# Optimization experiments

Measured on AMD Instinct MI355X. Metric: run time of the kernel, lower is better.

## Reference

```python
import jax, jax.numpy as jnp
import numpy as np

P = 8192  # num_particles
C = 8192  # num EEG channels (must equal P for the original broadcast to be valid)


def setup_inputs() -> dict:
    key = jax.random.key(0)
    k1, k2, k3, k4, k5 = jax.random.split(key, 5)
    inputs = jax.random.normal(k1, (1, C, P), dtype=jnp.float32)
    state_vector = jax.random.normal(k2, (P, 3), dtype=jnp.float32)
    # near-identity transition for numerical sanity
    transition_matrix = jnp.eye(3, dtype=jnp.float32) + 0.01 * jax.random.normal(k3, (3, 3), dtype=jnp.float32)
    # symmetric positive-definite process noise covariance (Cholesky must succeed)
    a = jax.random.normal(k4, (3, 3), dtype=jnp.float32)
    process_noise_cov = 0.01 * (a @ a.T) + 0.1 * jnp.eye(3, dtype=jnp.float32)
    forward_matrix = jax.random.normal(k5, (C, 3), dtype=jnp.float32)
    return {
        "inputs": inputs,
        "state_vector": state_vector,
        "transition_matrix": transition_matrix,
        "process_noise_cov": process_noise_cov,
        "forward_matrix": forward_matrix,
    }


def reference(inputs, state_vector, transition_matrix, process_noise_cov, forward_matrix):
    k_noise, k_cat = jax.random.split(jax.random.key(42))
    # --- state transition: x_new = x @ T^T + eps,  eps ~ N(0, Q) via z @ chol(Q) ---
    updated = state_vector @ transition_matrix.T                      # (P, 3)
    L = jnp.linalg.cholesky(process_noise_cov)                        # (3, 3) lower
    z = jax.random.normal(k_noise, (P, 3), dtype=state_vector.dtype)
    state = updated + z @ L                                           # (P, 3)
    # --- EEG measurement model: H @ x^T -> (C, P) ---
    predicted = forward_matrix @ state.T                              # (C, P)
    # --- particle weights: squared-residual sum (broadcast (1,C,P) - (P,C), C==P) ---
    w = jnp.sum(jnp.square(inputs - predicted.T), axis=-1)[0]         # (P,)
    # --- categorical resampling on log-weights (unnormalized logits) ---
    idx = jax.random.categorical(k_cat, jnp.log(w), shape=(P,))       # (P,) int
    resampled = state[idx]                                            # (P, 3) gather
    return jnp.mean(resampled, axis=0)                                # (3,)
```

## Files before the change

### kernel.cpp

```cpp
#include <hip/hip_runtime.h>
#include <stdint.h>

#define NP 8192
#define NC 8192

__host__ __device__ inline uint32_t rotl32(uint32_t x, int r) {
  return (x << r) | (x >> (32 - r));
}

__host__ __device__ inline void threefry2x32(uint32_t k0, uint32_t k1,
                                             uint32_t x0, uint32_t x1,
                                             uint32_t& o0, uint32_t& o1) {
  uint32_t ks2 = k0 ^ k1 ^ 0x1BD11BDAu;
  x0 += k0; x1 += k1;
#define TF_R(r) { x0 += x1; x1 = rotl32(x1, (r)); x1 ^= x0; }
  TF_R(13) TF_R(15) TF_R(26) TF_R(6)   x0 += k1;  x1 += ks2 + 1u;
  TF_R(17) TF_R(29) TF_R(16) TF_R(24)  x0 += ks2; x1 += k0 + 2u;
  TF_R(13) TF_R(15) TF_R(26) TF_R(6)   x0 += k0;  x1 += k1 + 3u;
  TF_R(17) TF_R(29) TF_R(16) TF_R(24)  x0 += k1;  x1 += ks2 + 4u;
  TF_R(13) TF_R(15) TF_R(26) TF_R(6)   x0 += ks2; x1 += k0 + 5u;
#undef TF_R
  o0 = x0; o1 = x1;
}

__device__ inline uint32_t tf_bits(uint32_t k0, uint32_t k1, uint32_t i) {
  uint32_t o0, o1;
  threefry2x32(k0, k1, 0u, i, o0, o1);
  return o0 ^ o1;
}

__device__ inline float u01(uint32_t bits) {
  return __uint_as_float((bits >> 9) | 0x3f800000u) - 1.0f;
}

__device__ inline float erfinvf_(float x) {
  float w = -log1pf(-x * x);
  float p;
  if (w < 5.0f) {
    w -= 2.5f;
    p = 2.81022636e-08f;
    p = fmaf(p, w, 3.43273939e-07f);
    p = fmaf(p, w, -3.5233877e-06f);
    p = fmaf(p, w, -4.39150654e-06f);
    p = fmaf(p, w, 0.00021858087f);
    p = fmaf(p, w, -0.00125372503f);
    p = fmaf(p, w, -0.00417768164f);
    p = fmaf(p, w, 0.246640727f);
    p = fmaf(p, w, 1.50140941f);
  } else {
    w = sqrtf(w) - 3.0f;
    p = -0.000200214257f;
    p = fmaf(p, w, 0.000100950558f);
    p = fmaf(p, w, 0.00134934322f);
    p = fmaf(p, w, -0.00367342844f);
    p = fmaf(p, w, 0.00573950773f);
    p = fmaf(p, w, -0.0076224613f);
    p = fmaf(p, w, 0.00943887047f);
    p = fmaf(p, w, 1.00167406f);
    p = fmaf(p, w, 2.83297682f);
  }
  return p * x;
}

__global__ void __launch_bounds__(256) k_normal(uint32_t k0, uint32_t k1, float* __restrict__ z) {
  uint32_t j = blockIdx.x * blockDim.x + threadIdx.x;
  if (j >= NP * 3) return;
  uint32_t bits = tf_bits(k0, k1, j);
  const float lo = -0.99999994f;
  float v = fmaxf(lo, u01(bits) * 2.0f + lo);
  z[j] = 1.41421356f * erfinvf_(v);
}

__global__ void __launch_bounds__(256) k_state(const float* __restrict__ sv,
                                               const float* __restrict__ T,
                                               const float* __restrict__ Q,
                                               const float* __restrict__ z,
                                               float* __restrict__ st) {
  int i = blockIdx.x * blockDim.x + threadIdx.x;
  if (i >= NP) return;
  float L00 = sqrtf(Q[0]);
  float L10 = Q[3] / L00, L20 = Q[6] / L00;
  float L11 = sqrtf(Q[4] - L10 * L10);
  float L21 = (Q[7] - L20 * L10) / L11;
  float L22 = sqrtf(Q[8] - L20 * L20 - L21 * L21);
  float s0 = sv[i * 3], s1 = sv[i * 3 + 1], s2 = sv[i * 3 + 2];
  float z0 = z[i * 3], z1 = z[i * 3 + 1], z2 = z[i * 3 + 2];
  float u0 = s0 * T[0] + s1 * T[1] + s2 * T[2];
  float u1 = s0 * T[3] + s1 * T[4] + s2 * T[5];
  float u2 = s0 * T[6] + s1 * T[7] + s2 * T[8];
  st[i * 3]     = u0 + (z0 * L00 + z1 * L10 + z2 * L20);
  st[i * 3 + 1] = u1 + (z1 * L11 + z2 * L21);
  st[i * 3 + 2] = u2 + (z2 * L22);
}

__global__ void __launch_bounds__(256) k_weights(const float* __restrict__ in,
                                                 const float* __restrict__ H,
                                                 const float* __restrict__ st,
                                                 float* __restrict__ logits) {
  int i = blockIdx.x;
  float s0 = st[i * 3], s1 = st[i * 3 + 1], s2 = st[i * 3 + 2];
  const float4* inrow = (const float4*)(in + (size_t)i * NC);
  const float4* H4 = (const float4*)H;
  float acc = 0.0f;
  for (int it = threadIdx.x; it < NC / 4; it += 256) {
    float4 x = inrow[it];
    float4 h0 = H4[it * 3 + 0];
    float4 h1 = H4[it * 3 + 1];
    float4 h2 = H4[it * 3 + 2];
    float p0 = h0.x * s0 + h0.y * s1 + h0.z * s2;
    float p1 = h0.w * s0 + h1.x * s1 + h1.y * s2;
    float p2 = h1.z * s0 + h1.w * s1 + h2.x * s2;
    float p3 = h2.y * s0 + h2.z * s1 + h2.w * s2;
    float d0 = x.x - p0, d1 = x.y - p1, d2 = x.z - p2, d3 = x.w - p3;
    acc += d0 * d0 + d1 * d1 + d2 * d2 + d3 * d3;
  }
  __shared__ float red[256];
  red[threadIdx.x] = acc;
  __syncthreads();
  for (int s = 128; s > 0; s >>= 1) {
    if (threadIdx.x < s) red[threadIdx.x] += red[threadIdx.x + s];
    __syncthreads();
  }
  if (threadIdx.x == 0) logits[i] = logf(red[0]);
}

__global__ void __launch_bounds__(256) k_resample(uint32_t k0, uint32_t k1,
                                                  const float* __restrict__ logits,
                                                  int* __restrict__ idx) {
  __shared__ float lg[NP];
  for (int t = threadIdx.x; t < NP; t += 256) lg[t] = logits[t];
  __syncthreads();
  uint32_t s = blockIdx.x;
  uint32_t base = s * (uint32_t)NP;
  const float TINY = 1.17549435e-38f;
  float b = -3.4e38f;
  int bi = 0;
  for (uint32_t i = threadIdx.x; i < NP; i += 256) {
    uint32_t bits = tf_bits(k0, k1, base + i);
    float v = fmaxf(TINY, u01(bits) * 1.0f + TINY);
    float g = -logf(-logf(v)) + lg[i];
    if (g > b) { b = g; bi = (int)i; }
  }
  __shared__ float rv[256];
  __shared__ int ri[256];
  rv[threadIdx.x] = b;
  ri[threadIdx.x] = bi;
  __syncthreads();
  for (int st = 128; st > 0; st >>= 1) {
    if (threadIdx.x < st) {
      float va = rv[threadIdx.x], vb = rv[threadIdx.x + st];
      int ia = ri[threadIdx.x], ib = ri[threadIdx.x + st];
      if (vb > va || (vb == va && ib < ia)) { rv[threadIdx.x] = vb; ri[threadIdx.x] = ib; }
    }
    __syncthreads();
  }
  if (threadIdx.x == 0) idx[s] = ri[0];
}

__global__ void __launch_bounds__(256) k_mean(const float* __restrict__ st,
                                              const int* __restrict__ idx,
                                              float* __restrict__ out) {
  double a0 = 0, a1 = 0, a2 = 0;
  for (int s = threadIdx.x; s < NP; s += 256) {
    int j = idx[s];
    a0 += st[j * 3];
    a1 += st[j * 3 + 1];
    a2 += st[j * 3 + 2];
  }
  __shared__ double r0[256], r1[256], r2[256];
  r0[threadIdx.x] = a0; r1[threadIdx.x] = a1; r2[threadIdx.x] = a2;
  __syncthreads();
  for (int s = 128; s > 0; s >>= 1) {
    if (threadIdx.x < s) {
      r0[threadIdx.x] += r0[threadIdx.x + s];
      r1[threadIdx.x] += r1[threadIdx.x + s];
      r2[threadIdx.x] += r2[threadIdx.x + s];
    }
    __syncthreads();
  }
  if (threadIdx.x == 0) {
    out[0] = (float)(r0[0] / NP);
    out[1] = (float)(r1[0] / NP);
    out[2] = (float)(r2[0] / NP);
  }
}

extern "C" void kernel_launch(void* const* d_in, const int* in_sizes, int n_in,
                              void* d_out, int out_size, void* d_ws, size_t ws_size,
                              hipStream_t stream) {
  const float* in = (const float*)d_in[0];
  const float* sv = (const float*)d_in[1];
  const float* T  = (const float*)d_in[2];
  const float* Q  = (const float*)d_in[3];
  const float* H  = (const float*)d_in[4];
  float* out = (float*)d_out;

  float* z      = (float*)d_ws;
  float* st     = z + 24576;
  float* logits = st + 24576;
  int*   idx    = (int*)(logits + NP);

  uint32_t nk0, nk1, ck0, ck1;
  threefry2x32(0u, 42u, 0u, 0u, nk0, nk1);
  threefry2x32(0u, 42u, 0u, 1u, ck0, ck1);

  hipLaunchKernelGGL(k_normal, dim3(96), dim3(256), 0, stream, nk0, nk1, z);
  hipLaunchKernelGGL(k_state, dim3(32), dim3(256), 0, stream, sv, T, Q, z, st);
  hipLaunchKernelGGL(k_weights, dim3(NP), dim3(256), 0, stream, in, H, st, logits);
  hipLaunchKernelGGL(k_resample, dim3(NP), dim3(256), 0, stream, ck0, ck1, logits, idx);
  hipLaunchKernelGGL(k_mean, dim3(1), dim3(256), 0, stream, st, idx, out);
}
```

Measured before the change: 596.6 us.

## Replace Gumbel-max resampling with exponential race and use wave-per-row weights

The resampling kernel no longer computes -log(-log(u)) + log(w) per draw. It uses the equivalent exponential-race form: the argmin over i of -log(u)/w_i, with 1/w precomputed by the weights kernel. This removes one of the two logs, makes the remaining one the fast __logf, and drops the per-row logf. The weights kernel now gives each 64-lane wave one row, reduced with shuffles instead of a shared-memory tree, and launches a quarter as many blocks. The argmin is mathematically equivalent, but rounding differences and the lower-precision __logf could flip selected indices relative to the reference.

After: 576.1 us. 1.04x faster.

```diff
diff --git a/kernel.cpp b/kernel.cpp
--- a/kernel.cpp
+++ b/kernel.cpp
@@ -96,13 +96,16 @@
 __global__ void __launch_bounds__(256) k_weights(const float* __restrict__ in,
                                                  const float* __restrict__ H,
                                                  const float* __restrict__ st,
-                                                 float* __restrict__ logits) {
-  int i = blockIdx.x;
-  float s0 = st[i * 3], s1 = st[i * 3 + 1], s2 = st[i * 3 + 2];
-  const float4* inrow = (const float4*)(in + (size_t)i * NC);
+                                                 float* __restrict__ winv) {
+  int wave = threadIdx.x >> 6;
+  int lane = threadIdx.x & 63;
+  int row = blockIdx.x * 4 + wave;
+  float s0 = st[row * 3], s1 = st[row * 3 + 1], s2 = st[row * 3 + 2];
+  const float4* inrow = (const float4*)(in + (size_t)row * NC);
   const float4* H4 = (const float4*)H;
   float acc = 0.0f;
-  for (int it = threadIdx.x; it < NC / 4; it += 256) {
+#pragma unroll 8
+  for (int it = lane; it < NC / 4; it += 64) {
     float4 x = inrow[it];
     float4 h0 = H4[it * 3 + 0];
     float4 h1 = H4[it * 3 + 1];
@@ -114,43 +117,40 @@
     float d0 = x.x - p0, d1 = x.y - p1, d2 = x.z - p2, d3 = x.w - p3;
     acc += d0 * d0 + d1 * d1 + d2 * d2 + d3 * d3;
   }
-  __shared__ float red[256];
-  red[threadIdx.x] = acc;
-  __syncthreads();
-  for (int s = 128; s > 0; s >>= 1) {
-    if (threadIdx.x < s) red[threadIdx.x] += red[threadIdx.x + s];
-    __syncthreads();
-  }
-  if (threadIdx.x == 0) logits[i] = logf(red[0]);
+#pragma unroll
+  for (int off = 32; off > 0; off >>= 1) acc += __shfl_down(acc, off, 64);
+  if (lane == 0) winv[row] = 1.0f / acc;
 }
 
 __global__ void __launch_bounds__(256) k_resample(uint32_t k0, uint32_t k1,
-                                                  const float* __restrict__ logits,
+                                                  const float* __restrict__ winv,
                                                   int* __restrict__ idx) {
-  __shared__ float lg[NP];
-  for (int t = threadIdx.x; t < NP; t += 256) lg[t] = logits[t];
+  __shared__ float wi[NP];
+  for (int t = threadIdx.x; t < NP; t += 256) wi[t] = winv[t];
   __syncthreads();
   uint32_t s = blockIdx.x;
   uint32_t base = s * (uint32_t)NP;
   const float TINY = 1.17549435e-38f;
-  float b = -3.4e38f;
+  float best = 3.4e38f;
   int bi = 0;
+#pragma unroll 4
   for (uint32_t i = threadIdx.x; i < NP; i += 256) {
     uint32_t bits = tf_bits(k0, k1, base + i);
-    float v = fmaxf(TINY, u01(bits) * 1.0f + TINY);
-    float g = -logf(-logf(v)) + lg[i];
-    if (g > b) { b = g; bi = (int)i; }
+    float v = fmaxf(TINY, u01(bits) + TINY);
+    float y = -__logf(v);
+    float r = y * wi[i];
+    if (r < best) { best = r; bi = (int)i; }
   }
   __shared__ float rv[256];
   __shared__ int ri[256];
-  rv[threadIdx.x] = b;
+  rv[threadIdx.x] = best;
   ri[threadIdx.x] = bi;
   __syncthreads();
-  for (int st = 128; st > 0; st >>= 1) {
-    if (threadIdx.x < st) {
-      float va = rv[threadIdx.x], vb = rv[threadIdx.x + st];
-      int ia = ri[threadIdx.x], ib = ri[threadIdx.x + st];
-      if (vb > va || (vb == va && ib < ia)) { rv[threadIdx.x] = vb; ri[threadIdx.x] = ib; }
+  for (int stp = 128; stp > 0; stp >>= 1) {
+    if (threadIdx.x < stp) {
+      float va = rv[threadIdx.x], vb = rv[threadIdx.x + stp];
+      int ia = ri[threadIdx.x], ib = ri[threadIdx.x + stp];
+      if (vb < va || (vb == va && ib < ia)) { rv[threadIdx.x] = vb; ri[threadIdx.x] = ib; }
     }
     __syncthreads();
   }
@@ -195,10 +195,10 @@
   const float* H  = (const float*)d_in[4];
   float* out = (float*)d_out;
 
-  float* z      = (float*)d_ws;
-  float* st     = z + 24576;
-  float* logits = st + 24576;
-  int*   idx    = (int*)(logits + NP);
+  float* z    = (float*)d_ws;
+  float* st   = z + 24576;
+  float* winv = st + 24576;
+  int*   idx  = (int*)(winv + NP);
 
   uint32_t nk0, nk1, ck0, ck1;
   threefry2x32(0u, 42u, 0u, 0u, nk0, nk1);
@@ -206,7 +206,7 @@
 
   hipLaunchKernelGGL(k_normal, dim3(96), dim3(256), 0, stream, nk0, nk1, z);
   hipLaunchKernelGGL(k_state, dim3(32), dim3(256), 0, stream, sv, T, Q, z, st);
-  hipLaunchKernelGGL(k_weights, dim3(NP), dim3(256), 0, stream, in, H, st, logits);
-  hipLaunchKernelGGL(k_resample, dim3(NP), dim3(256), 0, stream, ck0, ck1, logits, idx);
+  hipLaunchKernelGGL(k_weights, dim3(NP / 4), dim3(256), 0, stream, in, H, st, winv);
+  hipLaunchKernelGGL(k_resample, dim3(NP), dim3(256), 0, stream, ck0, ck1, winv, idx);
   hipLaunchKernelGGL(k_mean, dim3(1), dim3(256), 0, stream, st, idx, out);
 }
```
